# Performance work log

Hardware: AMD Instinct MI355X
Metric: run time of the kernel (lower is better)

## Reference

```python
import jax, jax.numpy as jnp
import numpy as np

B, N, D = 16, 8192, 64
M, S = 256, 32          # npoints, nsample
OUT = 128
RADIUS = 0.4
WC = 64                 # WeightNet output channels
BN_EPS = 1e-5
_BN_SCALE = 1.0 / np.sqrt(1.0 + BN_EPS)  # eval-mode BN, running mean 0 / var 1


def _bn(x, gamma, beta):
    shp = [1] * x.ndim
    shp[1] = -1
    return gamma.reshape(shp) * (x * _BN_SCALE) + beta.reshape(shp)


def _pdist2(a, b):
    # a (B,P,3), b (B,Q,3) -> (B,P,Q) squared distances
    return (jnp.sum(a * a, -1)[:, :, None] + jnp.sum(b * b, -1)[:, None, :]
            - 2.0 * jnp.einsum('bpd,bqd->bpq', a, b))


def _fps(xyz, npoints):
    # furthest point sampling, pointnet2 semantics (start at index 0)
    Bq, Nq, _ = xyz.shape
    first = jnp.zeros((Bq,), jnp.int32)

    def step(carry, _):
        dist, last = carry
        pt = xyz[jnp.arange(Bq), last]                   # (B,3)
        d = jnp.sum((xyz - pt[:, None, :]) ** 2, -1)
        dist = jnp.minimum(dist, d)
        nxt = jnp.argmax(dist, -1).astype(jnp.int32)
        return (dist, nxt), nxt

    init = (jnp.full((Bq, Nq), 1e10, xyz.dtype), first)
    _, rest = jax.lax.scan(step, init, None, length=npoints - 1)
    return jnp.concatenate([first[None], rest], 0).T     # (B, npoints)


def _ball_query(xyz, new_xyz, radius, nsample):
    # first `nsample` indices within radius, pad by repeating first valid index
    d2 = _pdist2(new_xyz, xyz)                           # (B,M,N)
    n = xyz.shape[1]
    key = jnp.where(d2 <= radius * radius, n - jnp.arange(n, dtype=jnp.int32), 0)
    vals, idx = jax.lax.top_k(key, nsample)              # lowest in-radius indices first
    return jnp.where(vals > 0, idx, idx[:, :, :1])


def _group(x_ch, idx):
    # x_ch (B,C,N), idx (B,M,S) -> (B,C,M,S)
    return jax.vmap(lambda f, i: f[:, i])(x_ch, idx)


def setup_inputs():
    key = jax.random.key(0)
    ks = jax.random.split(key, 8)
    f = jnp.float32

    def w(k, o, i):
        return (jax.random.normal(k, (o, i), f) / np.sqrt(i)).astype(f)

    return {
        'xyz': jax.random.uniform(ks[0], (B, N, 3), f),
        'feature': jax.random.normal(ks[1], (B, D, N), f),
        'w0': w(ks[2], WC, 3), 'b0': jnp.zeros((WC,), f), 'gamma0': jnp.ones((WC,), f), 'beta0': jnp.zeros((WC,), f),
        'w1': w(ks[3], WC, WC), 'b1': jnp.zeros((WC,), f), 'gamma1': jnp.ones((WC,), f), 'beta1': jnp.zeros((WC,), f),
        'w2': w(ks[4], WC, WC), 'b2': jnp.zeros((WC,), f),
        'wl': w(ks[5], OUT, D * WC), 'bl': jnp.zeros((OUT,), f), 'gammal': jnp.ones((OUT,), f), 'betal': jnp.zeros((OUT,), f),
        'wf': w(ks[6], OUT, D + OUT), 'bf': jnp.zeros((OUT,), f), 'gammaf': jnp.ones((OUT,), f), 'betaf': jnp.zeros((OUT,), f),
    }


def reference(xyz, feature, w0, b0, gamma0, beta0, w1, b1, gamma1, beta1, w2, b2,
              wl, bl, gammal, betal, wf, bf, gammaf, betaf):
    relu = jax.nn.relu
    # ---- furthest point sampling ----
    fidx = _fps(xyz, M)                                  # (B,M)
    new_xyz = xyz[jnp.arange(B)[:, None], fidx]          # (B,M,3)
    # ---- ball query + grouping ----
    gidx = _ball_query(xyz, new_xyz, RADIUS, S)          # (B,M,S)
    xyz_ch = jnp.transpose(xyz, (0, 2, 1))               # (B,3,N)
    grouped_xyz = _group(xyz_ch, gidx) - jnp.transpose(new_xyz, (0, 2, 1))[:, :, :, None]  # (B,3,M,S) centered
    grouped_feat = _group(feature, gidx)                 # (B,D,M,S)
    # ---- WeightNet (1x1 convs on offsets) ----
    h = relu(_bn(jnp.einsum('oc,bcms->boms', w0, grouped_xyz) + b0[None, :, None, None], gamma0, beta0))
    h = relu(_bn(jnp.einsum('oc,bcms->boms', w1, h) + b1[None, :, None, None], gamma1, beta1))
    weights = jnp.einsum('oc,bcms->boms', w2, h) + b2[None, :, None, None]  # (B,WC,M,S)
    # ---- weighted aggregation: (B,M,D,S) @ (B,M,S,WC) -> (B,M,D*WC) ----
    agg = jnp.einsum('bdms,bwms->bmdw', grouped_feat, weights).reshape(B, M, D * WC)
    new_feature = relu(_bn(jnp.einsum('od,bmd->bom', wl, agg) + bl[None, :, None], gammal, betal))  # (B,OUT,M)
    # ---- three-NN interpolation back to N points ----
    d2 = _pdist2(xyz, new_xyz)                           # (B,N,M)
    negd, nidx = jax.lax.top_k(-d2, 3)                   # 3 nearest sampled centers
    rd = 1.0 / (-negd + 1e-8)                            # reverse density on squared distance
    wts = rd / jnp.sum(rd, -1, keepdims=True)            # (B,N,3)
    gathered = jax.vmap(lambda f2, i: f2[:, i])(new_feature, nidx)  # (B,OUT,N,3)
    interp = jnp.einsum('bcnk,bnk->bcn', gathered, wts)  # (B,OUT,N)
    # ---- concat skip + final 1x1 conv ----
    cat = jnp.concatenate([interp, feature], 1)          # (B,OUT+D,N)
    return relu(_bn(jnp.einsum('oc,bcn->bon', wf, cat) + bf[None, :, None], gammaf, betaf))
```

## Files before the change

kernel.cpp:

```cpp
#include <hip/hip_runtime.h>
#include <hip/hip_bf16.h>
#include <cstdint>
#include <cstddef>

#define BB   16
#define NN   8192
#define DD   64
#define MM   256
#define SS   32
#define OUTC 128
#define WCC  64

using short8 = __attribute__((ext_vector_type(8))) short;
using f32x4  = __attribute__((ext_vector_type(4))) float;

__device__ __forceinline__ float bnf(float x, float g, float be){
    const float BNS = 0.99999500003749969f;
    return g * (x * BNS) + be;
}
__device__ __forceinline__ unsigned short f2bf(float f){
    __hip_bfloat16 h = __float2bfloat16(f);
    return *reinterpret_cast<unsigned short*>(&h);
}
__device__ __forceinline__ float bf2f(unsigned short u){
    return __uint_as_float(((unsigned)u) << 16);
}

#define PRE_GRID (16 + 2048 + 512 + 24)

__global__ __launch_bounds__(256, 1) void k_pre(const float* __restrict__ xyz, float* __restrict__ nxyz,
    const float* __restrict__ feature, unsigned short* __restrict__ featB,
    const float* __restrict__ wl, unsigned short* __restrict__ wlB,
    const float* __restrict__ wf, unsigned short* __restrict__ wfB){
  __shared__ union {
    struct {
      float sxyz[NN*3];
      float snew[MM*3];
      unsigned long long skey[2][4];
    } f;
    float tile[64][65];
  } sm;
  const int t = threadIdx.x;
  int blk = blockIdx.x;

  if (blk < 16){
    const int b = blk;
    const float* xb = xyz + (size_t)b*NN*3;
    for (int i = t; i < NN*3; i += 256) sm.f.sxyz[i] = xb[i];
    float px[32], py[32], pz[32], pn[32], dist[32];
#pragma unroll
    for (int i=0;i<32;i++){
      const int id = i*256 + t;
      px[i] = xb[id*3+0]; py[i] = xb[id*3+1]; pz[i] = xb[id*3+2];
      pn[i] = px[i]*px[i] + py[i]*py[i] + pz[i]*pz[i];
      dist[i] = 1e10f;
    }
    __syncthreads();
    float lx = sm.f.sxyz[0], ly = sm.f.sxyz[1], lz = sm.f.sxyz[2];
    if (t==0){ sm.f.snew[0]=lx; sm.f.snew[1]=ly; sm.f.snew[2]=lz; }
    for (int step=1; step<MM; ++step){
      const float nlx = -2.0f*lx, nly = -2.0f*ly, nlz = -2.0f*lz;
      const float l2s = lx*lx + ly*ly + lz*lz;
      float bv = 0.0f; int bil = 0;
#pragma unroll
      for (int i=0;i<32;i++){
        float c  = pn[i] + l2s;
        float d  = __builtin_fmaf(px[i], nlx, __builtin_fmaf(py[i], nly, __builtin_fmaf(pz[i], nlz, c)));
        float nd = fminf(dist[i], d);
        dist[i] = nd;
        bool gt = nd > bv;
        bv  = gt ? nd : bv;
        bil = gt ? i  : bil;
      }
      const int bi = bil*256 + t;
      unsigned long long key = ((unsigned long long)__float_as_uint(bv) << 32) | (unsigned)(NN-1 - bi);
#define DPP_U64_MAX(CTRL) do { \
        unsigned lo_ = (unsigned)key, hi_ = (unsigned)(key >> 32); \
        unsigned olo_ = (unsigned)__builtin_amdgcn_update_dpp((int)lo_, (int)lo_, (CTRL), 0xF, 0xF, 0); \
        unsigned ohi_ = (unsigned)__builtin_amdgcn_update_dpp((int)hi_, (int)hi_, (CTRL), 0xF, 0xF, 0); \
        unsigned long long ok_ = ((unsigned long long)ohi_ << 32) | olo_; \
        key = ok_ > key ? ok_ : key; \
      } while(0)
      DPP_U64_MAX(0x111);
      DPP_U64_MAX(0x112);
      DPP_U64_MAX(0x114);
      DPP_U64_MAX(0x118);
      DPP_U64_MAX(0x142);
      DPP_U64_MAX(0x143);
#undef DPP_U64_MAX
      {
        unsigned klo = (unsigned)__builtin_amdgcn_readlane((int)(unsigned)key, 63);
        unsigned khi = (unsigned)__builtin_amdgcn_readlane((int)(unsigned)(key >> 32), 63);
        key = ((unsigned long long)khi << 32) | klo;
      }
      const int p = step & 1;
      if ((t & 63) == 0) sm.f.skey[p][t>>6] = key;
      __syncthreads();
      unsigned long long k0=sm.f.skey[p][0], k1=sm.f.skey[p][1], k2=sm.f.skey[p][2], k3=sm.f.skey[p][3];
      unsigned long long ka = k0>k1?k0:k1, kb = k2>k3?k2:k3;
      unsigned long long kw = ka>kb?ka:kb;
      const int bid = (NN-1) - (int)(unsigned)(kw & 0xFFFFFFFFull);
      lx = sm.f.sxyz[bid*3+0]; ly = sm.f.sxyz[bid*3+1]; lz = sm.f.sxyz[bid*3+2];
      if (t==0){ sm.f.snew[step*3+0]=lx; sm.f.snew[step*3+1]=ly; sm.f.snew[step*3+2]=lz; }
    }
    __syncthreads();
    for (int i = t; i < MM*3; i += 256) nxyz[(size_t)b*MM*3 + i] = sm.f.snew[i];
    return;
  }
  blk -= 16;
  if (blk < 2048){
    const int b  = blk >> 7;
    const int n0 = (blk & 127) << 6;
    {
      const int d = t >> 2, j0 = (t & 3) << 4;
      const float* src = feature + ((size_t)b*DD + d)*NN + n0 + j0;
#pragma unroll
      for (int i=0;i<16;i+=4){
        float4 v = *(const float4*)(src + i);
        sm.tile[d][j0+i+0]=v.x; sm.tile[d][j0+i+1]=v.y; sm.tile[d][j0+i+2]=v.z; sm.tile[d][j0+i+3]=v.w;
      }
    }
    __syncthreads();
    {
      const int j = t >> 2, d0 = (t & 3) << 4;
      unsigned short hv[16];
#pragma unroll
      for (int i=0;i<16;i++) hv[i] = f2bf(sm.tile[d0+i][j]);
      unsigned short* dst = featB + ((size_t)b*NN + n0 + j)*64 + d0;
      *(uint4*)(dst)     = *(uint4*)(&hv[0]);
      *(uint4*)(dst + 8) = *(uint4*)(&hv[8]);
    }
    return;
  }
  blk -= 2048;
  if (blk < 512){
    int idx = (blk*256 + t)*4;
    float4 v = *(const float4*)(wl + idx);
    ushort4 h = make_ushort4(f2bf(v.x), f2bf(v.y), f2bf(v.z), f2bf(v.w));
    *(ushort4*)(wlB + idx) = h;
    return;
  }
  blk -= 512;
  {
    int idx = (blk*256 + t)*4;
    if (idx < 128*192){
      float4 v = *(const float4*)(wf + idx);
      ushort4 h = make_ushort4(f2bf(v.x), f2bf(v.y), f2bf(v.z), f2bf(v.w));
      *(ushort4*)(wfB + idx) = h;
    }
  }
}

__global__ __launch_bounds__(64) void k_bq_mlp(const float* __restrict__ xyz,
    const float* __restrict__ nxyz,
    const float* __restrict__ w0, const float* __restrict__ b0,
    const float* __restrict__ g0, const float* __restrict__ be0,
    const float* __restrict__ w1, const float* __restrict__ b1,
    const float* __restrict__ g1, const float* __restrict__ be1,
    const float* __restrict__ w2, const float* __restrict__ b2,
    int* __restrict__ gidx, float* __restrict__ wbuf){
  const int bm = blockIdx.x;
  const int b  = bm >> 8;
  const int c  = threadIdx.x;
  __shared__ int   sidx[SS];
  __shared__ float sgx[3][SS];
  __shared__ float sh0[SS][WCC];
  __shared__ float sh1[SS][WCC];

  const float w0r0 = w0[c*3+0], w0r1 = w0[c*3+1], w0r2 = w0[c*3+2];
  const float b0c=b0[c], g0c=g0[c], be0c=be0[c];
  const float b1c=b1[c], g1c=g1[c], be1c=be1[c], b2c=b2[c];
  float w1r[64], w2r[64];
#pragma unroll
  for (int i=0;i<16;i++){
    float4 v = *(const float4*)(w1 + c*64 + i*4);
    w1r[i*4+0]=v.x; w1r[i*4+1]=v.y; w1r[i*4+2]=v.z; w1r[i*4+3]=v.w;
    float4 u = *(const float4*)(w2 + c*64 + i*4);
    w2r[i*4+0]=u.x; w2r[i*4+1]=u.y; w2r[i*4+2]=u.z; w2r[i*4+3]=u.w;
  }
  const float cx = nxyz[bm*3+0], cy = nxyz[bm*3+1], cz = nxyz[bm*3+2];
  const float* xb = xyz + (size_t)b*NN*3;
  const float R2 = (float)(0.4*0.4);
  int cnt = 0;
  for (int n0=0; n0<NN && cnt<SS; n0+=64){
    int n = n0 + c;
    float dx = xb[n*3+0]-cx, dy = xb[n*3+1]-cy, dz = xb[n*3+2]-cz;
    float d2 = dx*dx+dy*dy+dz*dz;
    bool in = (d2 <= R2);
    unsigned long long mk = __ballot(in);
    int rank = cnt + (int)__popcll(mk & ((1ull<<c)-1ull));
    if (in && rank < SS) sidx[rank] = n;
    cnt += (int)__popcll(mk);
  }
  int total = min(cnt, SS);
  __syncthreads();
  int i0 = sidx[0];
  if (c >= total && c < SS) sidx[c] = i0;
  __syncthreads();
  if (c < SS){
    int p = sidx[c];
    gidx[bm*SS + c] = p;
    sgx[0][c] = xb[p*3+0]-cx;
    sgx[1][c] = xb[p*3+1]-cy;
    sgx[2][c] = xb[p*3+2]-cz;
  }
  __syncthreads();
  for (int s=0;s<SS;s++){
    float pre = w0r0*sgx[0][s] + w0r1*sgx[1][s] + w0r2*sgx[2][s] + b0c;
    sh0[s][c] = fmaxf(bnf(pre, g0c, be0c), 0.f);
  }
  __syncthreads();
  for (int s=0;s<SS;s++){
    float a = b1c;
#pragma unroll
    for (int k=0;k<64;k+=4){
      float4 h = *(const float4*)(&sh0[s][k]);
      a += w1r[k]*h.x + w1r[k+1]*h.y + w1r[k+2]*h.z + w1r[k+3]*h.w;
    }
    sh1[s][c] = fmaxf(bnf(a, g1c, be1c), 0.f);
  }
  __syncthreads();
  float* wb = wbuf + (size_t)bm*SS*WCC;
  for (int s=0;s<SS;s++){
    float a = b2c;
#pragma unroll
    for (int k=0;k<64;k+=4){
      float4 h = *(const float4*)(&sh1[s][k]);
      a += w2r[k]*h.x + w2r[k+1]*h.y + w2r[k+2]*h.z + w2r[k+3]*h.w;
    }
    wb[s*WCC + c] = a;
  }
}

__global__ __launch_bounds__(256) void k_agg(const unsigned short* __restrict__ featB,
                                             const float* __restrict__ wbuf,
                                             const int* __restrict__ gidx,
                                             unsigned short* __restrict__ aggB){
  const int bm = blockIdx.x;
  const int b  = bm >> 8;
  __shared__ float wt[SS][WCC];
  __shared__ int   sidx[SS];
  const int t = threadIdx.x;
  const float* wsrc = wbuf + (size_t)bm*SS*WCC;
#pragma unroll
  for (int i=0;i<8;i++){
    int li = t + i*256;
    ((float*)wt)[li] = wsrc[li];
  }
  if (t < SS) sidx[t] = gidx[bm*SS + t];
  __syncthreads();
  const int d  = t & 63;
  const int wg = t >> 6;
  float acc[16];
#pragma unroll
  for (int j=0;j<16;j++) acc[j]=0.f;
  const unsigned short* fb = featB + (size_t)b*NN*64;
  for (int s=0;s<SS;s++){
    float fv = bf2f(fb[(size_t)sidx[s]*64 + d]);
#pragma unroll
    for (int j=0;j<16;j++) acc[j] += fv * wt[s][wg*16+j];
  }
  unsigned short h[16];
#pragma unroll
  for (int j=0;j<16;j++) h[j] = f2bf(acc[j]);
  unsigned short* ab = aggB + (size_t)bm*4096 + d*64 + wg*16;
  *(uint4*)(ab)     = *(uint4*)(&h[0]);
  *(uint4*)(ab + 8) = *(uint4*)(&h[8]);
}

__global__ __launch_bounds__(256) void k_nf_part(const unsigned short* __restrict__ aggB,
                                                 const unsigned short* __restrict__ wlB,
                                                 float* __restrict__ part){
  const int blk = blockIdx.x;
  const int rb  = blk >> 3;
  const int ks  = blk & 7;
  const int wid = threadIdx.x >> 6, lane = threadIdx.x & 63;
  const int m0 = rb*64 + wid*16;
  const int r  = lane & 15, kg = lane >> 4;
  f32x4 acc[8];
#pragma unroll
  for (int i=0;i<8;i++) acc[i] = (f32x4){0.f,0.f,0.f,0.f};
  const short* arow = (const short*)aggB + (size_t)(m0 + r)*4096 + ks*512 + kg*8;
  const short* brow = (const short*)wlB  + (size_t)r*4096        + ks*512 + kg*8;
#pragma unroll 4
  for (int kc=0; kc<16; kc++){
    short8 a = *(const short8*)(arow + kc*32);
#pragma unroll
    for (int ot=0; ot<8; ot++){
      short8 bfr = *(const short8*)(brow + (size_t)ot*16*4096 + kc*32);
      acc[ot] = __builtin_amdgcn_mfma_f32_16x16x32_bf16(a, bfr, acc[ot], 0, 0, 0);
    }
  }
  float* pb = part + ((size_t)ks << 19);
#pragma unroll
  for (int ot=0; ot<8; ot++){
#pragma unroll
    for (int rr=0; rr<4; rr++){
      int row = m0 + kg*4 + rr;
      pb[(size_t)row*128 + ot*16 + r] = acc[ot][rr];
    }
  }
}

__global__ __launch_bounds__(256) void k_nf_ep(const float* __restrict__ part,
    const float* __restrict__ bl, const float* __restrict__ gl, const float* __restrict__ bel,
    float* __restrict__ nfT){
  const int gid = blockIdx.x*256 + threadIdx.x;
  const int base = gid*4;
  const int o0 = base & 127;
  float sum[4] = {0.f, 0.f, 0.f, 0.f};
#pragma unroll
  for (int s=0;s<8;s++){
    float4 v = *(const float4*)(part + ((size_t)s<<19) + base);
    sum[0]+=v.x; sum[1]+=v.y; sum[2]+=v.z; sum[3]+=v.w;
  }
  float ov[4];
#pragma unroll
  for (int j=0;j<4;j++){
    const int o = o0 + j;
    ov[j] = fmaxf(bnf(sum[j] + bl[o], gl[o], bel[o]), 0.f);
  }
  *(float4*)(nfT + base) = make_float4(ov[0],ov[1],ov[2],ov[3]);
}

__global__ __launch_bounds__(256) void k_final(const float* __restrict__ xyz,
    const float* __restrict__ nxyz, const float* __restrict__ nfT,
    const unsigned short* __restrict__ featB, const unsigned short* __restrict__ wfB,
    const float* __restrict__ bf, const float* __restrict__ gf, const float* __restrict__ bef,
    float* __restrict__ out){
  const int blk = blockIdx.x;
  const int b  = blk >> 6;
  const int n0 = (blk & 63) << 7;
  __shared__ float snew[MM*3];
  __shared__ float sw[128][3];
  __shared__ int   si[128][3];
  const int t = threadIdx.x;
  if (t < 192){
    float4 v = *(const float4*)(nxyz + (size_t)b*MM*3 + t*4);
    snew[t*4+0]=v.x; snew[t*4+1]=v.y; snew[t*4+2]=v.z; snew[t*4+3]=v.w;
  }
  __syncthreads();
  if (t < 128){
    const int n = n0 + t;
    const float x = xyz[((size_t)b*NN+n)*3+0];
    const float y = xyz[((size_t)b*NN+n)*3+1];
    const float z = xyz[((size_t)b*NN+n)*3+2];
    float d1=1e30f, d2=1e30f, d3=1e30f; int i1=0,i2=0,i3=0;
    for (int m=0;m<MM;m++){
      float dx=x-snew[m*3+0], dy=y-snew[m*3+1], dz=z-snew[m*3+2];
      float d = dx*dx+dy*dy+dz*dz;
      if (d < d3){
        if (d < d1){ d3=d2;i3=i2; d2=d1;i2=i1; d1=d;i1=m; }
        else if (d < d2){ d3=d2;i3=i2; d2=d;i2=m; }
        else { d3=d;i3=m; }
      }
    }
    float r1=1.f/(d1+1e-8f), r2=1.f/(d2+1e-8f), r3=1.f/(d3+1e-8f);
    float rs = 1.f/(r1+r2+r3);
    sw[t][0]=r1*rs; sw[t][1]=r2*rs; sw[t][2]=r3*rs;
    si[t][0]=i1; si[t][1]=i2; si[t][2]=i3;
  }
  __syncthreads();

  const int w = t >> 6, lane = t & 63;
  const int r = lane & 15, kg = lane >> 4;
  float wA[8][3]; int iA[8][3];
#pragma unroll
  for (int nt=0;nt<8;nt++){
    int n = nt*16 + r;
    wA[nt][0]=sw[n][0]; wA[nt][1]=sw[n][1]; wA[nt][2]=sw[n][2];
    iA[nt][0]=si[n][0]*128; iA[nt][1]=si[n][1]*128; iA[nt][2]=si[n][2]*128;
  }
  const float* nfb = nfT + (size_t)b*MM*128;
  const unsigned short* fbB = featB + ((size_t)b*NN + n0)*64;
  const unsigned short* wfRow0 = wfB + (size_t)(w*32 +      r)*192 + kg*8;
  const unsigned short* wfRow1 = wfB + (size_t)(w*32 + 16 + r)*192 + kg*8;
  f32x4 acc[2][8];
#pragma unroll
  for (int i=0;i<2;i++)
#pragma unroll
    for (int j=0;j<8;j++) acc[i][j] = (f32x4){0.f,0.f,0.f,0.f};

#pragma unroll
  for (int c=0;c<6;c++){
    short8 a0 = *(const short8*)(wfRow0 + c*32);
    short8 a1 = *(const short8*)(wfRow1 + c*32);
    if (c < 4){
      const int k8 = c*32 + kg*8;
#pragma unroll
      for (int nt=0;nt<8;nt++){
        const float* p0 = nfb + iA[nt][0] + k8;
        const float* p1 = nfb + iA[nt][1] + k8;
        const float* p2 = nfb + iA[nt][2] + k8;
        float4 xa = *(const float4*)(p0), xb4 = *(const float4*)(p0+4);
        float4 ya = *(const float4*)(p1), yb4 = *(const float4*)(p1+4);
        float4 za = *(const float4*)(p2), zb4 = *(const float4*)(p2+4);
        const float w0v=wA[nt][0], w1v=wA[nt][1], w2v=wA[nt][2];
        float e0 = w0v*xa.x + w1v*ya.x + w2v*za.x;
        float e1 = w0v*xa.y + w1v*ya.y + w2v*za.y;
        float e2 = w0v*xa.z + w1v*ya.z + w2v*za.z;
        float e3 = w0v*xa.w + w1v*ya.w + w2v*za.w;
        float e4 = w0v*xb4.x + w1v*yb4.x + w2v*zb4.x;
        float e5 = w0v*xb4.y + w1v*yb4.y + w2v*zb4.y;
        float e6 = w0v*xb4.z + w1v*yb4.z + w2v*zb4.z;
        float e7 = w0v*xb4.w + w1v*yb4.w + w2v*zb4.w;
        short8 bfr = { (short)f2bf(e0), (short)f2bf(e1), (short)f2bf(e2), (short)f2bf(e3),
                       (short)f2bf(e4), (short)f2bf(e5), (short)f2bf(e6), (short)f2bf(e7) };
        acc[0][nt] = __builtin_amdgcn_mfma_f32_16x16x32_bf16(a0, bfr, acc[0][nt], 0, 0, 0);
        acc[1][nt] = __builtin_amdgcn_mfma_f32_16x16x32_bf16(a1, bfr, acc[1][nt], 0, 0, 0);
      }
    } else {
      const int d8 = (c-4)*32 + kg*8;
#pragma unroll
      for (int nt=0;nt<8;nt++){
        short8 bfr = *(const short8*)(fbB + (size_t)(nt*16 + r)*64 + d8);
        acc[0][nt] = __builtin_amdgcn_mfma_f32_16x16x32_bf16(a0, bfr, acc[0][nt], 0, 0, 0);
        acc[1][nt] = __builtin_amdgcn_mfma_f32_16x16x32_bf16(a1, bfr, acc[1][nt], 0, 0, 0);
      }
    }
  }
#pragma unroll
  for (int ot=0; ot<2; ot++){
#pragma unroll
    for (int rr=0; rr<4; rr++){
      const int o = w*32 + ot*16 + kg*4 + rr;
      const float bfo = bf[o], gfo = gf[o], befo = bef[o];
      float* dst = out + ((size_t)b*OUTC + o)*NN + n0 + r;
#pragma unroll
      for (int nt=0;nt<8;nt++){
        float val = fmaxf(bnf(acc[ot][nt][rr] + bfo, gfo, befo), 0.f);
        dst[nt*16] = val;
      }
    }
  }
}

extern "C" void kernel_launch(void* const* d_in, const int* in_sizes, int n_in,
                              void* d_out, int out_size, void* d_ws, size_t ws_size,
                              hipStream_t stream){
  const float* xyz     = (const float*)d_in[0];
  const float* feature = (const float*)d_in[1];
  const float* w0  = (const float*)d_in[2];
  const float* b0  = (const float*)d_in[3];
  const float* g0  = (const float*)d_in[4];
  const float* be0 = (const float*)d_in[5];
  const float* w1  = (const float*)d_in[6];
  const float* b1  = (const float*)d_in[7];
  const float* g1  = (const float*)d_in[8];
  const float* be1 = (const float*)d_in[9];
  const float* w2  = (const float*)d_in[10];
  const float* b2  = (const float*)d_in[11];
  const float* wl  = (const float*)d_in[12];
  const float* bl  = (const float*)d_in[13];
  const float* gl  = (const float*)d_in[14];
  const float* bel = (const float*)d_in[15];
  const float* wf  = (const float*)d_in[16];
  const float* bf  = (const float*)d_in[17];
  const float* gf  = (const float*)d_in[18];
  const float* bef = (const float*)d_in[19];
  float* out = (float*)d_out;

  char* ws = (char*)d_ws;
  unsigned short* featB = (unsigned short*)(ws + 0);
  float*          wbuf  = (float*)(ws + 16777216);
  float*          part  = (float*)(ws + 16777216);
  unsigned short* aggB  = (unsigned short*)(ws + 50331648);
  unsigned short* wlB   = (unsigned short*)(ws + 83886080);
  unsigned short* wfB   = (unsigned short*)(ws + 84934656);
  float*          nxyz  = (float*)(ws + 84983808);
  int*            gidx  = (int*)  (ws + 85032960);
  float*          nfT   = (float*)(ws + 85557248);

  k_pre    <<<PRE_GRID, 256, 0, stream>>>(xyz, nxyz, feature, featB, wl, wlB, wf, wfB);
  k_bq_mlp <<<BB*MM, 64, 0, stream>>>(xyz, nxyz, w0,b0,g0,be0, w1,b1,g1,be1, w2,b2, gidx, wbuf);
  k_agg    <<<BB*MM, 256, 0, stream>>>(featB, wbuf, gidx, aggB);
  k_nf_part<<<512,  256, 0, stream>>>(aggB, wlB, part);
  k_nf_ep  <<<512,  256, 0, stream>>>(part, bl, gl, bel, nfT);
  k_final  <<<BB*(NN/128), 256, 0, stream>>>(xyz, nxyz, nfT, featB, wfB, bf, gf, bef, out);
}
```

Measured before the change: 559.0 us.

## Fuse ball query, WeightNet MLP and aggregation into one 256-thread kernel

Merges the ball-query/WeightNet kernel and the aggregation kernel into one block per center, so the per-sample weights stay in shared memory instead of making a round trip through a global buffer. The ball query is split across four waves, each scanning a quarter of the points, and the partial lists are concatenated in index order. The MLP layers are also spread across the four waves instead of a single 64-thread wave. The cost is higher per-block register and shared-memory use from the held weight rows and extra buffers, plus some wasted scanning in the later quarters.

```diff
diff --git a/kernel.cpp b/kernel.cpp
--- a/kernel.cpp
+++ b/kernel.cpp
@@ -151,21 +151,27 @@
   }
 }
 
-__global__ __launch_bounds__(64) void k_bq_mlp(const float* __restrict__ xyz,
+__global__ __launch_bounds__(256) void k_group(const float* __restrict__ xyz,
     const float* __restrict__ nxyz,
     const float* __restrict__ w0, const float* __restrict__ b0,
     const float* __restrict__ g0, const float* __restrict__ be0,
     const float* __restrict__ w1, const float* __restrict__ b1,
     const float* __restrict__ g1, const float* __restrict__ be1,
     const float* __restrict__ w2, const float* __restrict__ b2,
-    int* __restrict__ gidx, float* __restrict__ wbuf){
+    const unsigned short* __restrict__ featB,
+    unsigned short* __restrict__ aggB){
   const int bm = blockIdx.x;
   const int b  = bm >> 8;
-  const int c  = threadIdx.x;
+  const int t  = threadIdx.x;
+  const int c  = t & 63;
+  const int wg = t >> 6;
+  __shared__ int   wlist[4][SS];
+  __shared__ int   wcnt[4];
   __shared__ int   sidx[SS];
   __shared__ float sgx[3][SS];
   __shared__ float sh0[SS][WCC];
   __shared__ float sh1[SS][WCC];
+  __shared__ float swt[SS][WCC];
 
   const float w0r0 = w0[c*3+0], w0r1 = w0[c*3+1], w0r2 = w0[c*3+2];
   const float b0c=b0[c], g0c=g0[c], be0c=be0[c];
@@ -181,36 +187,48 @@
   const float cx = nxyz[bm*3+0], cy = nxyz[bm*3+1], cz = nxyz[bm*3+2];
   const float* xb = xyz + (size_t)b*NN*3;
   const float R2 = (float)(0.4*0.4);
-  int cnt = 0;
-  for (int n0=0; n0<NN && cnt<SS; n0+=64){
-    int n = n0 + c;
-    float dx = xb[n*3+0]-cx, dy = xb[n*3+1]-cy, dz = xb[n*3+2]-cz;
-    float d2 = dx*dx+dy*dy+dz*dz;
-    bool in = (d2 <= R2);
-    unsigned long long mk = __ballot(in);
-    int rank = cnt + (int)__popcll(mk & ((1ull<<c)-1ull));
-    if (in && rank < SS) sidx[rank] = n;
-    cnt += (int)__popcll(mk);
-  }
-  int total = min(cnt, SS);
-  __syncthreads();
-  int i0 = sidx[0];
-  if (c >= total && c < SS) sidx[c] = i0;
-  __syncthreads();
-  if (c < SS){
-    int p = sidx[c];
-    gidx[bm*SS + c] = p;
-    sgx[0][c] = xb[p*3+0]-cx;
-    sgx[1][c] = xb[p*3+1]-cy;
-    sgx[2][c] = xb[p*3+2]-cz;
-  }
-  __syncthreads();
-  for (int s=0;s<SS;s++){
+
+  {
+    int cnt = 0;
+    const int base = wg*2048;
+    for (int n0=0; n0<2048 && cnt<SS; n0+=64){
+      int n = base + n0 + c;
+      float dx = xb[n*3+0]-cx, dy = xb[n*3+1]-cy, dz = xb[n*3+2]-cz;
+      float d2 = dx*dx+dy*dy+dz*dz;
+      bool in = (d2 <= R2);
+      unsigned long long mk = __ballot(in);
+      int rank = cnt + (int)__popcll(mk & ((1ull<<c)-1ull));
+      if (in && rank < SS) wlist[wg][rank] = n;
+      cnt += (int)__popcll(mk);
+    }
+    if (c==0) wcnt[wg] = min(cnt, SS);
+  }
+  __syncthreads();
+  if (t < SS){
+    const int c0=wcnt[0], c1=wcnt[1], c2=wcnt[2], c3=wcnt[3];
+    const int a1=c0+c1, a2=a1+c2, a3=a2+c3;
+    int idx;
+    if      (t < c0) idx = wlist[0][t];
+    else if (t < a1) idx = wlist[1][t-c0];
+    else if (t < a2) idx = wlist[2][t-a1];
+    else if (t < a3) idx = wlist[3][t-a2];
+    else idx = (c0>0) ? wlist[0][0] : (c1>0) ? wlist[1][0] : (c2>0) ? wlist[2][0] : wlist[3][0];
+    sidx[t] = idx;
+    sgx[0][t] = xb[idx*3+0]-cx;
+    sgx[1][t] = xb[idx*3+1]-cy;
+    sgx[2][t] = xb[idx*3+2]-cz;
+  }
+  __syncthreads();
+#pragma unroll
+  for (int i=0;i<8;i++){
+    const int s = i*4 + wg;
     float pre = w0r0*sgx[0][s] + w0r1*sgx[1][s] + w0r2*sgx[2][s] + b0c;
     sh0[s][c] = fmaxf(bnf(pre, g0c, be0c), 0.f);
   }
   __syncthreads();
-  for (int s=0;s<SS;s++){
+#pragma unroll
+  for (int i=0;i<8;i++){
+    const int s = i*4 + wg;
     float a = b1c;
 #pragma unroll
     for (int k=0;k<64;k+=4){
@@ -220,37 +238,19 @@
     sh1[s][c] = fmaxf(bnf(a, g1c, be1c), 0.f);
   }
   __syncthreads();
-  float* wb = wbuf + (size_t)bm*SS*WCC;
-  for (int s=0;s<SS;s++){
+#pragma unroll
+  for (int i=0;i<8;i++){
+    const int s = i*4 + wg;
     float a = b2c;
 #pragma unroll
     for (int k=0;k<64;k+=4){
       float4 h = *(const float4*)(&sh1[s][k]);
       a += w2r[k]*h.x + w2r[k+1]*h.y + w2r[k+2]*h.z + w2r[k+3]*h.w;
     }
-    wb[s*WCC + c] = a;
-  }
-}
-
-__global__ __launch_bounds__(256) void k_agg(const unsigned short* __restrict__ featB,
-                                             const float* __restrict__ wbuf,
-                                             const int* __restrict__ gidx,
-                                             unsigned short* __restrict__ aggB){
-  const int bm = blockIdx.x;
-  const int b  = bm >> 8;
-  __shared__ float wt[SS][WCC];
-  __shared__ int   sidx[SS];
-  const int t = threadIdx.x;
-  const float* wsrc = wbuf + (size_t)bm*SS*WCC;
-#pragma unroll
-  for (int i=0;i<8;i++){
-    int li = t + i*256;
-    ((float*)wt)[li] = wsrc[li];
-  }
-  if (t < SS) sidx[t] = gidx[bm*SS + t];
-  __syncthreads();
-  const int d  = t & 63;
-  const int wg = t >> 6;
+    swt[s][c] = a;
+  }
+  __syncthreads();
+  const int d = c;
   float acc[16];
 #pragma unroll
   for (int j=0;j<16;j++) acc[j]=0.f;
@@ -258,7 +258,7 @@
   for (int s=0;s<SS;s++){
     float fv = bf2f(fb[(size_t)sidx[s]*64 + d]);
 #pragma unroll
-    for (int j=0;j<16;j++) acc[j] += fv * wt[s][wg*16+j];
+    for (int j=0;j<16;j++) acc[j] += fv * swt[s][wg*16+j];
   }
   unsigned short h[16];
 #pragma unroll
@@ -462,18 +462,15 @@
 
   char* ws = (char*)d_ws;
   unsigned short* featB = (unsigned short*)(ws + 0);
-  float*          wbuf  = (float*)(ws + 16777216);
   float*          part  = (float*)(ws + 16777216);
   unsigned short* aggB  = (unsigned short*)(ws + 50331648);
   unsigned short* wlB   = (unsigned short*)(ws + 83886080);
   unsigned short* wfB   = (unsigned short*)(ws + 84934656);
   float*          nxyz  = (float*)(ws + 84983808);
-  int*            gidx  = (int*)  (ws + 85032960);
   float*          nfT   = (float*)(ws + 85557248);
 
   k_pre    <<<PRE_GRID, 256, 0, stream>>>(xyz, nxyz, feature, featB, wl, wlB, wf, wfB);
-  k_bq_mlp <<<BB*MM, 64, 0, stream>>>(xyz, nxyz, w0,b0,g0,be0, w1,b1,g1,be1, w2,b2, gidx, wbuf);
-  k_agg    <<<BB*MM, 256, 0, stream>>>(featB, wbuf, gidx, aggB);
+  k_group  <<<BB*MM, 256, 0, stream>>>(xyz, nxyz, w0,b0,g0,be0, w1,b1,g1,be1, w2,b2, featB, aggB);
   k_nf_part<<<512,  256, 0, stream>>>(aggB, wlB, part);
   k_nf_ep  <<<512,  256, 0, stream>>>(part, bl, gl, bel, nfT);
   k_final  <<<BB*(NN/128), 256, 0, stream>>>(xyz, nxyz, nfT, featB, wfB, bf, gf, bef, out);
```

New measurement: 565.3 us. No clear change (+1.1%).
